# Kernel tuning notes

Hardware: AMD Instinct MI355X
Metric: run time of the kernel (lower is better)

Reference implementation:

```python
import jax, jax.numpy as jnp
import numpy as np

N_HEADS = 16

def setup_inputs() -> dict:
    key = jax.random.key(0)
    ks = jax.random.split(key, 6)
    B, S, D = 2, 2048, 1024
    sc = 0.02
    return {
        "x": jax.random.normal(ks[0], (B, S, D), dtype=jnp.float32),
        "Wq": jax.random.normal(ks[1], (D, D), dtype=jnp.float32) * sc,
        "Wk": jax.random.normal(ks[2], (D, D), dtype=jnp.float32) * sc,
        "Wv": jax.random.normal(ks[3], (D, D), dtype=jnp.float32) * sc,
        "Wo": jax.random.normal(ks[4], (D, D), dtype=jnp.float32) * sc,
        "bo": jnp.zeros((D,), dtype=jnp.float32),
        "stride": 64,
    }

def _strided_mask(S: int, stride: int):
    # local window |i-j|<=1  OR  |i-j| == k*stride (k>=1); diff==0 is in the window
    i = jnp.arange(S)[:, None]
    j = jnp.arange(S)[None, :]
    diff = jnp.abs(i - j)
    return (diff <= 1) | (diff % stride == 0)  # [S, S] bool

def reference(x, Wq, Wk, Wv, Wo, bo, stride):
    B, S, D = x.shape
    H = N_HEADS
    Dh = D // H
    # q/k/v projections: nn.Linear(bias=False) applies x @ W.T
    def proj(W):
        return (x @ W.T).reshape(B, S, H, Dh).transpose(0, 2, 1, 3)  # [B,H,S,Dh]
    q, k, v = proj(Wq), proj(Wk), proj(Wv)
    scores = jnp.einsum('bhqd,bhkd->bhqk', q, k) / jnp.sqrt(jnp.float32(Dh))
    mask = _strided_mask(S, stride)  # [S,S]
    scores = jnp.where(mask[None, None], scores, -jnp.inf)
    attn = jax.nn.softmax(scores, axis=-1)  # dropout is identity in eval
    out = jnp.einsum('bhqk,bhkd->bhqd', attn, v)  # [B,H,S,Dh]
    out = out.transpose(0, 2, 1, 3).reshape(B, S, D)
    return out @ Wo.T + bo
```

## Files before the change

kernel.cpp:

```cpp
#include <hip/hip_runtime.h>
#include <hip/hip_bf16.h>


typedef __bf16 bf16;
typedef __attribute__((ext_vector_type(4))) __bf16 bf16x4;
typedef __attribute__((ext_vector_type(8))) __bf16 bf16x8;
typedef __attribute__((ext_vector_type(4))) float f32x4;
typedef __attribute__((ext_vector_type(4))) unsigned int u32x4;

constexpr int S_ = 2048;
constexpr int D_ = 1024;
constexpr int H_ = 16;
constexpr int DH = 64;
constexpr int M_ = 2 * S_;

__device__ __forceinline__ void gload_lds16(const bf16* g, bf16* l) {
    __builtin_amdgcn_global_load_lds(
        (const __attribute__((address_space(1))) void*)g,
        (__attribute__((address_space(3))) void*)l, 16, 0, 0);
}

#define BARRIER_FULL() do { asm volatile("" ::: "memory"); \
    __builtin_amdgcn_sched_barrier(0); \
    __builtin_amdgcn_s_barrier(); \
    __builtin_amdgcn_sched_barrier(0); \
    asm volatile("" ::: "memory"); } while (0)

#define WAIT_LGKM0() do { asm volatile("s_waitcnt lgkmcnt(0)" ::: "memory"); \
    __builtin_amdgcn_sched_barrier(0); } while (0)

#define WAIT_VM0() do { asm volatile("s_waitcnt vmcnt(0)" ::: "memory"); \
    __builtin_amdgcn_sched_barrier(0); } while (0)

#define WAIT_VM4() do { asm volatile("s_waitcnt vmcnt(4)" ::: "memory"); \
    __builtin_amdgcn_sched_barrier(0); } while (0)

__device__ __forceinline__ void stage64(const bf16* __restrict__ G, int base_row,
                                        int kcol, bf16* lds, int wave, int lane)
{
    const int rIn = lane >> 3;
    const int g   = (lane & 7) ^ rIn;
    #pragma unroll
    for (int l = 0; l < 2; ++l) {
        const int c = wave * 2 + l;
        gload_lds16(G + (size_t)(base_row + c * 8 + rIn) * D_ + kcol + g * 8,
                    lds + c * 512);
    }
}

__global__ __launch_bounds__(512, 1)
void gemm_qkv_8p(const bf16* __restrict__ A,
                 const bf16* __restrict__ W,
                 bf16* __restrict__ C)
{
    constexpr int BK = 64;
    constexpr int NT = D_ / BK;
    constexpr int HS = 128 * BK;
    __shared__ __align__(16) bf16 As[2][2][HS];
    __shared__ __align__(16) bf16 Bs[2][2][HS];

    const int tid  = threadIdx.x;
    const int wave = tid >> 6;
    const int lane = tid & 63;
    const int wm = wave >> 2;
    const int wn = wave & 3;

    const int lid = blockIdx.y * 12 + blockIdx.x;
    const int xcd = lid & 7, pos = lid >> 3;
    const int bxs = (xcd & 1) * 6 + pos % 6;
    const int bys = (xcd >> 1) * 4 + pos / 6;
    const int bm = bys * 256;
    const int bn = bxs * 256;

    const int l15 = lane & 15;
    const int hi  = lane >> 4;
    const int r7  = l15 & 7;
    const int bh  = wn >> 1;

    int aOff[2][4][2], bOff[2][2][2];
    #pragma unroll
    for (int mh = 0; mh < 2; ++mh)
        #pragma unroll
        for (int fm = 0; fm < 4; ++fm)
            #pragma unroll
            for (int kk = 0; kk < 2; ++kk)
                aOff[mh][fm][kk] = (mh * 64 + fm * 16 + l15) * 64
                                 + (((kk * 4 + hi) ^ r7) * 8);
    #pragma unroll
    for (int nh = 0; nh < 2; ++nh)
        #pragma unroll
        for (int fn = 0; fn < 2; ++fn)
            #pragma unroll
            for (int kk = 0; kk < 2; ++kk)
                bOff[nh][fn][kk] = ((wn & 1) * 64 + nh * 32 + fn * 16 + l15) * 64
                                 + (((kk * 4 + hi) ^ r7) * 8);

    f32x4 acc[8][4];
    #pragma unroll
    for (int i = 0; i < 8; ++i)
        #pragma unroll
        for (int j = 0; j < 4; ++j) acc[i][j] = f32x4{0.f, 0.f, 0.f, 0.f};

    bf16x8 aF[4][2], bF0[2][2], bF1[2][2];

#define Q16(MH, NH, BF) do { _Pragma("unroll") \
    for (int fm = 0; fm < 4; ++fm) { _Pragma("unroll") \
        for (int fn = 0; fn < 2; ++fn) { _Pragma("unroll") \
            for (int kk = 0; kk < 2; ++kk) \
                acc[(MH)*4+fm][(NH)*2+fn] = __builtin_amdgcn_mfma_f32_16x16x32_bf16( \
                    aF[fm][kk], BF[fn][kk], acc[(MH)*4+fm][(NH)*2+fn], 0, 0, 0); \
    } } } while (0)

    stage64(A, bm +   0, 0,  &As[0][0][0], wave, lane);
    stage64(A, bm + 128, 0,  &As[0][1][0], wave, lane);
    stage64(W, bn +   0, 0,  &Bs[0][0][0], wave, lane);
    stage64(W, bn + 128, 0,  &Bs[0][1][0], wave, lane);
    stage64(W, bn +   0, BK, &Bs[1][0][0], wave, lane);
    stage64(A, bm +   0, BK, &As[1][0][0], wave, lane);
    WAIT_VM4();
    BARRIER_FULL();

    for (int t = 0; t < NT; ++t) {
        const int d = t & 1;
        const bf16* aH = &As[d][wm][0];
        const bf16* bH = &Bs[d][bh][0];
        const bool pre1 = (t + 1) < NT;
        const bool pre2 = (t + 2) < NT;
        const int k1 = (t + 1) * BK, k2 = (t + 2) * BK;

        #pragma unroll
        for (int fn = 0; fn < 2; ++fn)
            #pragma unroll
            for (int kk = 0; kk < 2; ++kk)
                bF0[fn][kk] = *(const bf16x8*)(bH + bOff[0][fn][kk]);
        #pragma unroll
        for (int fm = 0; fm < 4; ++fm)
            #pragma unroll
            for (int kk = 0; kk < 2; ++kk)
                aF[fm][kk] = *(const bf16x8*)(aH + aOff[0][fm][kk]);
        if (pre1) stage64(A, bm + 128, k1, &As[d ^ 1][1][0], wave, lane);
        BARRIER_FULL(); WAIT_LGKM0();
        __builtin_amdgcn_s_setprio(1); Q16(0, 0, bF0); __builtin_amdgcn_s_setprio(0);
        BARRIER_FULL();

        #pragma unroll
        for (int fn = 0; fn < 2; ++fn)
            #pragma unroll
            for (int kk = 0; kk < 2; ++kk)
                bF1[fn][kk] = *(const bf16x8*)(bH + bOff[1][fn][kk]);
        if (pre1) stage64(W, bn + 128, k1, &Bs[d ^ 1][1][0], wave, lane);
        BARRIER_FULL(); WAIT_LGKM0();
        __builtin_amdgcn_s_setprio(1); Q16(0, 1, bF1); __builtin_amdgcn_s_setprio(0);
        BARRIER_FULL();

        #pragma unroll
        for (int fm = 0; fm < 4; ++fm)
            #pragma unroll
            for (int kk = 0; kk < 2; ++kk)
                aF[fm][kk] = *(const bf16x8*)(aH + aOff[1][fm][kk]);
        if (pre2) stage64(W, bn + 0, k2, &Bs[d][0][0], wave, lane);
        BARRIER_FULL(); WAIT_LGKM0();
        __builtin_amdgcn_s_setprio(1); Q16(1, 1, bF1); __builtin_amdgcn_s_setprio(0);
        BARRIER_FULL();

        if (pre2) stage64(A, bm + 0, k2, &As[d][0][0], wave, lane);
        __builtin_amdgcn_s_setprio(1); Q16(1, 0, bF0); __builtin_amdgcn_s_setprio(0);
        if (pre2) { WAIT_VM4(); } else { WAIT_VM0(); }
        BARRIER_FULL();
    }
#undef Q16

    #pragma unroll
    for (int i = 0; i < 8; ++i) {
        #pragma unroll
        for (int j = 0; j < 4; ++j) {
            const int n = bn + wn * 64 + j * 16 + l15;
            bf16* Cz = C + (size_t)(n >> 10) * M_ * D_;
            const int col = n & 1023;
            const int mb = bm + wm * 128 + i * 16 + hi * 4;
            #pragma unroll
            for (int r2 = 0; r2 < 4; ++r2)
                Cz[(size_t)(mb + r2) * D_ + col] = (bf16)acc[i][j][r2];
        }
    }
}

__global__ __launch_bounds__(512, 1)
void gemm_o_2ph(const bf16* __restrict__ A,
                const bf16* __restrict__ W,
                float* __restrict__ Cf,
                const float* __restrict__ bias)
{
    constexpr int BK = 64;
    constexpr int NT = D_ / BK;
    constexpr int TSLOT = 128 * BK;
    __shared__ __align__(16) bf16 As[3 * TSLOT];
    __shared__ __align__(16) bf16 Bs[3 * TSLOT];

    const int tid  = threadIdx.x;
    const int wave = tid >> 6;
    const int lane = tid & 63;
    const int wm = wave >> 2;
    const int wn = wave & 3;

    const int lid = blockIdx.y * 8 + blockIdx.x;
    const int xcd = lid & 7, pos = lid >> 3;
    const int bxs = (xcd & 3) * 2 + (pos & 1);
    const int bys = (xcd >> 2) * 16 + (pos >> 1);
    const int bm = bys * 128;
    const int bn = bxs * 128;

    const int l15 = lane & 15;
    const int hi  = lane >> 4;
    const int r7  = l15 & 7;

    int aOff[2][4], bOff[2][2];
    #pragma unroll
    for (int ks = 0; ks < 2; ++ks) {
        #pragma unroll
        for (int fm = 0; fm < 4; ++fm)
            aOff[ks][fm] = (wm * 64 + fm * 16 + l15) * 64 + (((ks * 4 + hi) ^ r7) * 8);
        #pragma unroll
        for (int fn = 0; fn < 2; ++fn)
            bOff[ks][fn] = (wn * 32 + fn * 16 + l15) * 64 + (((ks * 4 + hi) ^ r7) * 8);
    }

    f32x4 acc[4][2];
    #pragma unroll
    for (int i = 0; i < 4; ++i)
        #pragma unroll
        for (int j = 0; j < 2; ++j) acc[i][j] = f32x4{0.f, 0.f, 0.f, 0.f};

    bf16x8 aF0[4], aF1[4], bF[2][2];

    stage64(A, bm, 0,  As,         wave, lane);
    stage64(W, bn, 0,  Bs,         wave, lane);
    stage64(A, bm, BK, As + TSLOT, wave, lane);
    stage64(W, bn, BK, Bs + TSLOT, wave, lane);
    WAIT_VM4();
    BARRIER_FULL();

    int cur = 0;
    for (int t = 0; t < NT; ++t) {
        const int ss = (cur + 2 >= 3) ? (cur - 1) : (cur + 2);
        const bf16* aslot = As + cur * TSLOT;
        const bf16* bslot = Bs + cur * TSLOT;
        const bool pre = (t + 2) < NT;
        const int kn = (t + 2) * BK;

        #pragma unroll
        for (int ks = 0; ks < 2; ++ks)
            #pragma unroll
            for (int fn = 0; fn < 2; ++fn)
                bF[ks][fn] = *(const bf16x8*)(bslot + bOff[ks][fn]);
        #pragma unroll
        for (int fm = 0; fm < 4; ++fm)
            aF0[fm] = *(const bf16x8*)(aslot + aOff[0][fm]);
        if (pre) stage64(A, bm, kn, As + ss * TSLOT, wave, lane);
        BARRIER_FULL(); WAIT_LGKM0();
        __builtin_amdgcn_s_setprio(1);
        #pragma unroll
        for (int fm = 0; fm < 4; ++fm)
            #pragma unroll
            for (int fn = 0; fn < 2; ++fn)
                acc[fm][fn] = __builtin_amdgcn_mfma_f32_16x16x32_bf16(
                    aF0[fm], bF[0][fn], acc[fm][fn], 0, 0, 0);
        __builtin_amdgcn_s_setprio(0);
        BARRIER_FULL();

        #pragma unroll
        for (int fm = 0; fm < 4; ++fm)
            aF1[fm] = *(const bf16x8*)(aslot + aOff[1][fm]);
        if (pre) stage64(W, bn, kn, Bs + ss * TSLOT, wave, lane);
        BARRIER_FULL(); WAIT_LGKM0();
        __builtin_amdgcn_s_setprio(1);
        #pragma unroll
        for (int fm = 0; fm < 4; ++fm)
            #pragma unroll
            for (int fn = 0; fn < 2; ++fn)
                acc[fm][fn] = __builtin_amdgcn_mfma_f32_16x16x32_bf16(
                    aF1[fm], bF[1][fn], acc[fm][fn], 0, 0, 0);
        __builtin_amdgcn_s_setprio(0);
        if (pre) { WAIT_VM4(); } else { WAIT_VM0(); }
        BARRIER_FULL();
        cur = (cur + 1 >= 3) ? 0 : (cur + 1);
    }

    #pragma unroll
    for (int fm = 0; fm < 4; ++fm) {
        #pragma unroll
        for (int fn = 0; fn < 2; ++fn) {
            const int n = bn + wn * 32 + fn * 16 + l15;
            const float bv = bias[n];
            const int mb = bm + wm * 64 + fm * 16 + hi * 4;
            #pragma unroll
            for (int r2 = 0; r2 < 4; ++r2)
                Cf[(size_t)(mb + r2) * D_ + n] = acc[fm][fn][r2] + bv;
        }
    }
}

template<bool AF32, bool BF32, bool CF32, bool BIAS>
__global__ __launch_bounds__(256)
void gemm_bt(const void* __restrict__ Av,
             const void* __restrict__ W0v, const void* __restrict__ W1v,
             const void* __restrict__ W2v,
             void* __restrict__ Cv, const float* __restrict__ bias)
{
    constexpr int BM = 128, BK = 64;
    constexpr int N = D_, K = D_;
    __shared__ __align__(16) bf16 As[BM * BK];
    __shared__ __align__(16) bf16 Bs[BM * BK];

    const int z = blockIdx.z;
    const void* Wv_ = (z == 0) ? W0v : (z == 1) ? W1v : W2v;

    const int tid  = threadIdx.x;
    const int wave = tid >> 6;
    const int lane = tid & 63;

    const int bm = blockIdx.y * BM;
    const int bn = blockIdx.x * BM;
    const int wr = wave >> 1;
    const int wc = wave & 1;

    f32x4 acc[4][4];
    #pragma unroll
    for (int i = 0; i < 4; ++i)
        #pragma unroll
        for (int j = 0; j < 4; ++j)
            acc[i][j] = f32x4{0.f, 0.f, 0.f, 0.f};

    const int ldRow = lane >> 3;
    const int ldCol = (lane & 7) * 8;

    for (int kt = 0; kt < K; kt += BK) {
        if (AF32) {
            const float* A = (const float*)Av;
            #pragma unroll
            for (int it = 0; it < 8; ++it) {
                const int flat = (it * 256 + tid) * 4;
                const int row = flat >> 6, col = flat & 63;
                const float4 v = *(const float4*)(A + (size_t)(bm + row) * K + kt + col);
                bf16x4 p = { (bf16)v.x, (bf16)v.y, (bf16)v.z, (bf16)v.w };
                *(bf16x4*)&As[row * BK + col] = p;
            }
        } else {
            const bf16* A = (const bf16*)Av;
            #pragma unroll
            for (int q = 0; q < 4; ++q) {
                const int c = wave * 4 + q;
                const int row = c * 8 + ldRow;
                gload_lds16(A + (size_t)(bm + row) * K + kt + ldCol, &As[c * 8 * BK]);
            }
        }
        if (BF32) {
            const float* W = (const float*)Wv_;
            #pragma unroll
            for (int it = 0; it < 8; ++it) {
                const int flat = (it * 256 + tid) * 4;
                const int row = flat >> 6, col = flat & 63;
                const float4 v = *(const float4*)(W + (size_t)(bn + row) * K + kt + col);
                bf16x4 p = { (bf16)v.x, (bf16)v.y, (bf16)v.z, (bf16)v.w };
                *(bf16x4*)&Bs[row * BK + col] = p;
            }
        } else {
            const bf16* W = (const bf16*)Wv_;
            #pragma unroll
            for (int q = 0; q < 4; ++q) {
                const int c = wave * 4 + q;
                const int row = c * 8 + ldRow;
                gload_lds16(W + (size_t)(bn + row) * K + kt + ldCol, &Bs[c * 8 * BK]);
            }
        }
        __syncthreads();
        #pragma unroll
        for (int kk = 0; kk < 2; ++kk) {
            const int k0 = kk * 32 + (lane >> 4) * 8;
            bf16x8 af[4], bfv[4];
            #pragma unroll
            for (int mi = 0; mi < 4; ++mi)
                af[mi] = *(const bf16x8*)&As[(wr * 64 + mi * 16 + (lane & 15)) * BK + k0];
            #pragma unroll
            for (int ni = 0; ni < 4; ++ni)
                bfv[ni] = *(const bf16x8*)&Bs[(wc * 64 + ni * 16 + (lane & 15)) * BK + k0];
            #pragma unroll
            for (int mi = 0; mi < 4; ++mi)
                #pragma unroll
                for (int ni = 0; ni < 4; ++ni)
                    acc[mi][ni] = __builtin_amdgcn_mfma_f32_16x16x32_bf16(
                        af[mi], bfv[ni], acc[mi][ni], 0, 0, 0);
        }
        __syncthreads();
    }

    #pragma unroll
    for (int mi = 0; mi < 4; ++mi) {
        #pragma unroll
        for (int ni = 0; ni < 4; ++ni) {
            const int n  = bn + wc * 64 + ni * 16 + (lane & 15);
            const int mb = bm + wr * 64 + mi * 16 + (lane >> 4) * 4;
            float bv = 0.f;
            if (BIAS) bv = bias[n];
            #pragma unroll
            for (int r2 = 0; r2 < 4; ++r2) {
                const int m = mb + r2;
                if (CF32) {
                    ((float*)Cv)[(size_t)m * N + n] = acc[mi][ni][r2] + bv;
                } else {
                    bf16* Cc = (bf16*)Cv + (size_t)z * M_ * D_;
                    Cc[(size_t)m * N + n] = (bf16)(acc[mi][ni][r2] + bv);
                }
            }
        }
    }
}

__global__ __launch_bounds__(256)
void convert_to_bf16(const float* __restrict__ x,
                     const float* __restrict__ w0, const float* __restrict__ w1,
                     const float* __restrict__ w2, const float* __restrict__ w3,
                     bf16* __restrict__ out)
{
    const size_t eid = ((size_t)blockIdx.x * 256 + threadIdx.x) * 8;
    const float* src; size_t off;
    if (eid < (size_t)(1u << 22)) { src = x; off = eid; }
    else {
        const size_t t = eid - (1u << 22);
        const int k = (int)(t >> 20);
        off = t & ((1u << 20) - 1);
        src = (k == 0) ? w0 : (k == 1) ? w1 : (k == 2) ? w2 : w3;
    }
    const float4 a = *(const float4*)(src + off);
    const float4 c = *(const float4*)(src + off + 4);
    bf16x8 v = { (bf16)a.x, (bf16)a.y, (bf16)a.z, (bf16)a.w,
                 (bf16)c.x, (bf16)c.y, (bf16)c.z, (bf16)c.w };
    *(bf16x8*)(out + eid) = v;
}

__device__ __forceinline__ unsigned pk2bf(float lo, float hi) {
    const unsigned a = __builtin_bit_cast(unsigned short, (bf16)lo);
    const unsigned b = __builtin_bit_cast(unsigned short, (bf16)hi);
    return a | (b << 16);
}

__global__ __launch_bounds__(256)
void attn_mfma(bf16* __restrict__ QA, const bf16* __restrict__ Kw,
               const bf16* __restrict__ Vw)
{
    const int lane = threadIdx.x & 63;
    const int wid  = blockIdx.x * 4 + (threadIdx.x >> 6);
    const int r = wid & 63;
    const int h = (wid >> 6) & (H_ - 1);
    const int b = wid >> 10;

    const int qlo = lane & 15;
    const int g   = lane >> 4;
    const size_t rb = (size_t)b * S_;
    const int col0 = h * DH;
    const float scale = 0.125f;

    f32x4 accS[2][2];
    #pragma unroll
    for (int a = 0; a < 2; ++a)
        #pragma unroll
        for (int c = 0; c < 2; ++c) accS[a][c] = f32x4{0.f,0.f,0.f,0.f};

    #pragma unroll
    for (int c = 0; c < 2; ++c) {
        bf16x8 kf[2], qf[2];
        #pragma unroll
        for (int t = 0; t < 2; ++t) {
            const size_t row = rb + (size_t)(r + 64 * (t * 16 + qlo));
            kf[t] = *(const bf16x8*)&Kw[row * D_ + col0 + c * 32 + g * 8];
            qf[t] = *(const bf16x8*)&QA[row * D_ + col0 + c * 32 + g * 8];
        }
        #pragma unroll
        for (int kt = 0; kt < 2; ++kt)
            #pragma unroll
            for (int qt = 0; qt < 2; ++qt)
                accS[kt][qt] = __builtin_amdgcn_mfma_f32_16x16x32_bf16(
                    kf[kt], qf[qt], accS[kt][qt], 0, 0, 0);
    }

    const int s_nb = lane & 31;
    const int side = lane >> 5;
    const int i_nb = r + 64 * s_nb;
    const int j_nb = side ? (i_nb + 1) : (i_nb - 1);
    const bool nbv = (unsigned)j_nb < (unsigned)S_;
    const int j_sf = nbv ? j_nb : i_nb;
    float nbd = 0.f;
    #pragma unroll
    for (int t = 0; t < 8; ++t) {
        const bf16x8 qv = *(const bf16x8*)&QA[(rb + i_nb) * D_ + col0 + t * 8];
        const bf16x8 kv = *(const bf16x8*)&Kw[(rb + j_sf) * D_ + col0 + t * 8];
        #pragma unroll
        for (int e = 0; e < 8; ++e) nbd += (float)qv[e] * (float)kv[e];
    }
    const float NEGINF = -__builtin_inff();
    float nb = nbv ? nbd * scale : NEGINF;

    float mx[2] = { NEGINF, NEGINF };
    #pragma unroll
    for (int kt = 0; kt < 2; ++kt)
        #pragma unroll
        for (int qt = 0; qt < 2; ++qt)
            #pragma unroll
            for (int rr = 0; rr < 4; ++rr)
                mx[qt] = fmaxf(mx[qt], accS[kt][qt][rr]);
    mx[0] *= scale; mx[1] *= scale;
    mx[g & 1] = fmaxf(mx[g & 1], nb);
    #pragma unroll
    for (int x = 16; x <= 32; x <<= 1) {
        mx[0] = fmaxf(mx[0], __shfl_xor(mx[0], x));
        mx[1] = fmaxf(mx[1], __shfl_xor(mx[1], x));
    }
    float p[2][2][4];
    float sm[2] = { 0.f, 0.f };
    #pragma unroll
    for (int kt = 0; kt < 2; ++kt)
        #pragma unroll
        for (int qt = 0; qt < 2; ++qt)
            #pragma unroll
            for (int rr = 0; rr < 4; ++rr) {
                const float e = __expf(accS[kt][qt][rr] * scale - mx[qt]);
                p[kt][qt][rr] = e;
                sm[qt] += e;
            }
    float nbp = __expf(nb - mx[g & 1]);
    sm[g & 1] += nbp;
    #pragma unroll
    for (int x = 16; x <= 32; x <<= 1) {
        sm[0] += __shfl_xor(sm[0], x);
        sm[1] += __shfl_xor(sm[1], x);
    }
    const float inv[2] = { 1.f / sm[0], 1.f / sm[1] };
    #pragma unroll
    for (int kt = 0; kt < 2; ++kt)
        #pragma unroll
        for (int qt = 0; qt < 2; ++qt)
            #pragma unroll
            for (int rr = 0; rr < 4; ++rr) p[kt][qt][rr] *= inv[qt];
    nbp *= inv[g & 1];

    unsigned pk_[2][2][2];
    #pragma unroll
    for (int qt = 0; qt < 2; ++qt)
        #pragma unroll
        for (int kt = 0; kt < 2; ++kt)
            #pragma unroll
            for (int w = 0; w < 2; ++w)
                pk_[qt][kt][w] = pk2bf(p[kt][qt][2 * w], p[kt][qt][2 * w + 1]);

    const int srcA = qlo + 32 * (g & 1);
    const int srcB = srcA + 16;
    const int kts  = g >> 1;
    bf16x8 pa[2];
    #pragma unroll
    for (int qt = 0; qt < 2; ++qt) {
        u32x4 fr;
        #pragma unroll
        for (int w = 0; w < 2; ++w) {
            const unsigned a0 = (unsigned)__shfl((int)pk_[qt][0][w], srcA);
            const unsigned a1 = (unsigned)__shfl((int)pk_[qt][1][w], srcA);
            fr[w] = kts ? a1 : a0;
            const unsigned b0 = (unsigned)__shfl((int)pk_[qt][0][w], srcB);
            const unsigned b1 = (unsigned)__shfl((int)pk_[qt][1][w], srcB);
            fr[2 + w] = kts ? b1 : b0;
        }
        pa[qt] = __builtin_bit_cast(bf16x8, fr);
    }

    f32x4 accO[2][4];
    #pragma unroll
    for (int qt = 0; qt < 2; ++qt)
        #pragma unroll
        for (int dt = 0; dt < 4; ++dt) accO[qt][dt] = f32x4{0.f,0.f,0.f,0.f};
    #pragma unroll
    for (int dt = 0; dt < 4; ++dt) {
        bf16x8 vf;
        #pragma unroll
        for (int e = 0; e < 8; ++e)
            vf[e] = Vw[(rb + (size_t)(r + 64 * (g * 8 + e))) * D_ + col0 + dt * 16 + qlo];
        accO[0][dt] = __builtin_amdgcn_mfma_f32_16x16x32_bf16(pa[0], vf, accO[0][dt], 0, 0, 0);
        accO[1][dt] = __builtin_amdgcn_mfma_f32_16x16x32_bf16(pa[1], vf, accO[1][dt], 0, 0, 0);
    }

    #pragma unroll
    for (int qt = 0; qt < 2; ++qt)
        #pragma unroll
        for (int rr = 0; rr < 4; ++rr) {
            const int q  = qt * 16 + g * 4 + rr;
            const int iq = r + 64 * q;
            const float pm = __shfl(nbp, q);
            const float pp = __shfl(nbp, q + 32);
            const int jm = iq > 0 ? iq - 1 : 0;
            const int jp = iq < S_ - 1 ? iq + 1 : S_ - 1;
            #pragma unroll
            for (int dt = 0; dt < 4; ++dt) {
                const int d = col0 + dt * 16 + qlo;
                const float vm = (float)Vw[(rb + jm) * D_ + d];
                const float vp = (float)Vw[(rb + jp) * D_ + d];
                const float o = accO[qt][dt][rr] + pm * vm + pp * vp;
                QA[(rb + iq) * D_ + d] = (bf16)o;
            }
        }
}

extern "C" void kernel_launch(void* const* d_in, const int* in_sizes, int n_in,
                              void* d_out, int out_size, void* d_ws, size_t ws_size,
                              hipStream_t stream)
{
    const float* x  = (const float*)d_in[0];
    const float* Wq = (const float*)d_in[1];
    const float* Wk = (const float*)d_in[2];
    const float* Wv = (const float*)d_in[3];
    const float* Wo = (const float*)d_in[4];
    const float* bo = (const float*)d_in[5];

    bf16* qws = (bf16*)d_ws;
    bf16* kws = qws + (size_t)M_ * D_;
    bf16* vws = kws + (size_t)M_ * D_;

    const bool fast = ws_size >= (size_t)40 * 1024 * 1024;

    if (fast) {
        bf16* xb  = vws + (size_t)M_ * D_;
        bf16* wqb = xb + (1u << 22);
        bf16* wob = wqb + 3 * (1u << 20);

        convert_to_bf16<<<4096, 256, 0, stream>>>(x, Wq, Wk, Wv, Wo, xb);

        gemm_qkv_8p<<<dim3(3 * D_ / 256, M_ / 256), 512, 0, stream>>>(xb, wqb, qws);

        attn_mfma<<<dim3(2 * H_ * 64 / 4), 256, 0, stream>>>(qws, kws, vws);

        gemm_o_2ph<<<dim3(D_ / 128, M_ / 128), 512, 0, stream>>>(
            qws, wob, (float*)d_out, bo);
    } else {
        gemm_bt<true, true, false, false><<<dim3(D_/128, M_/128, 3), 256, 0, stream>>>(
            x, Wq, Wk, Wv, qws, nullptr);

        attn_mfma<<<dim3(2 * H_ * 64 / 4), 256, 0, stream>>>(qws, kws, vws);

        gemm_bt<false, true, true, true><<<dim3(D_/128, M_/128, 1), 256, 0, stream>>>(
            qws, Wo, nullptr, nullptr, (float*)d_out, bo);
    }
}
```

Baseline: 85.83 us.

## Stage V tile in LDS via async loads and bounce output through LDS

The strided-key V rows for each wave are now prefetched asynchronously into a per-wave, XOR-swizzled LDS slot at kernel start, overlapping the score computation. The B fragments are then read from LDS instead of as scattered 2-byte global loads. The output epilogue writes the accumulators to an LDS bounce buffer so each row is stored and its neighbour-V terms are loaded as contiguous 64-lane coalesced accesses. This adds about 49KB of shared memory per block, which may reduce occupancy, and the epilogue is now a 32-iteration serial loop.

```diff
diff --git a/kernel.cpp b/kernel.cpp
--- a/kernel.cpp
+++ b/kernel.cpp
@@ -448,8 +448,12 @@
 void attn_mfma(bf16* __restrict__ QA, const bf16* __restrict__ Kw,
                const bf16* __restrict__ Vw)
 {
+    constexpr int WSLOT = 4096 + 8320;
+    __shared__ __align__(16) unsigned char smem[4 * WSLOT];
+
     const int lane = threadIdx.x & 63;
-    const int wid  = blockIdx.x * 4 + (threadIdx.x >> 6);
+    const int wv   = threadIdx.x >> 6;
+    const int wid  = blockIdx.x * 4 + wv;
     const int r = wid & 63;
     const int h = (wid >> 6) & (H_ - 1);
     const int b = wid >> 10;
@@ -459,6 +463,22 @@
     const size_t rb = (size_t)b * S_;
     const int col0 = h * DH;
     const float scale = 0.125f;
+
+    unsigned char* ws = smem + wv * WSLOT;
+    bf16*  vlds = (bf16*)ws;
+    float* bnce = (float*)(ws + 4096);
+
+    {
+        const int krow = lane >> 3;
+        const int slot = lane & 7;
+        #pragma unroll
+        for (int i = 0; i < 4; ++i) {
+            const int k = i * 8 + krow;
+            gload_lds16(Vw + (rb + (size_t)(r + 64 * k)) * D_ + col0
+                           + ((slot ^ (k & 7)) * 8),
+                        vlds + i * 512);
+        }
+    }
 
     f32x4 accS[2][2];
     #pragma unroll
@@ -571,6 +591,7 @@
         pa[qt] = __builtin_bit_cast(bf16x8, fr);
     }
 
+    WAIT_VM0();
     f32x4 accO[2][4];
     #pragma unroll
     for (int qt = 0; qt < 2; ++qt)
@@ -579,9 +600,15 @@
     #pragma unroll
     for (int dt = 0; dt < 4; ++dt) {
         bf16x8 vf;
-        #pragma unroll
-        for (int e = 0; e < 8; ++e)
-            vf[e] = Vw[(rb + (size_t)(r + 64 * (g * 8 + e))) * D_ + col0 + dt * 16 + qlo];
+        const int sbase = dt * 2 + (qlo >> 3);
+        const int boff  = (qlo & 7) * 2;
+        #pragma unroll
+        for (int e = 0; e < 8; ++e) {
+            const int k = g * 8 + e;
+            const unsigned short u = *(const unsigned short*)
+                ((const unsigned char*)vlds + k * 128 + ((sbase ^ (k & 7)) * 16) + boff);
+            vf[e] = __builtin_bit_cast(bf16, u);
+        }
         accO[0][dt] = __builtin_amdgcn_mfma_f32_16x16x32_bf16(pa[0], vf, accO[0][dt], 0, 0, 0);
         accO[1][dt] = __builtin_amdgcn_mfma_f32_16x16x32_bf16(pa[1], vf, accO[1][dt], 0, 0, 0);
     }
@@ -590,21 +617,24 @@
     for (int qt = 0; qt < 2; ++qt)
         #pragma unroll
         for (int rr = 0; rr < 4; ++rr) {
-            const int q  = qt * 16 + g * 4 + rr;
-            const int iq = r + 64 * q;
-            const float pm = __shfl(nbp, q);
-            const float pp = __shfl(nbp, q + 32);
-            const int jm = iq > 0 ? iq - 1 : 0;
-            const int jp = iq < S_ - 1 ? iq + 1 : S_ - 1;
-            #pragma unroll
-            for (int dt = 0; dt < 4; ++dt) {
-                const int d = col0 + dt * 16 + qlo;
-                const float vm = (float)Vw[(rb + jm) * D_ + d];
-                const float vp = (float)Vw[(rb + jp) * D_ + d];
-                const float o = accO[qt][dt][rr] + pm * vm + pp * vp;
-                QA[(rb + iq) * D_ + d] = (bf16)o;
-            }
-        }
+            const int q = qt * 16 + g * 4 + rr;
+            #pragma unroll
+            for (int dt = 0; dt < 4; ++dt)
+                bnce[q * 65 + dt * 16 + qlo] = accO[qt][dt][rr];
+        }
+    WAIT_LGKM0();
+
+    for (int q = 0; q < 32; ++q) {
+        const float pm = __shfl(nbp, q);
+        const float pp = __shfl(nbp, q + 32);
+        const int iq = r + 64 * q;
+        const int jm = iq > 0 ? iq - 1 : 0;
+        const int jp = iq < S_ - 1 ? iq + 1 : S_ - 1;
+        float o = bnce[q * 65 + lane];
+        o += pm * (float)Vw[(rb + jm) * D_ + col0 + lane];
+        o += pp * (float)Vw[(rb + jp) * D_ + col0 + lane];
+        QA[(rb + iq) * D_ + col0 + lane] = (bf16)o;
+    }
 }
 
 extern "C" void kernel_launch(void* const* d_in, const int* in_sizes, int n_in,
```

New measurement: 84.62 us. About the same (-1.4%).
